# Kernel tuning notes

Hardware: AMD Instinct MI355X
Metric: run time of the kernel (lower is better)

## Reference

```python
import jax, jax.numpy as jnp
import numpy as np
from jax import lax

SQRT2 = 1.4142135623730951
NEG_SLOPE = 0.2


def _haar_kernels():
    l = np.ones((1, 2), np.float32) / np.float32(np.sqrt(2.0))
    h = l.copy()
    h[0, 0] = -h[0, 0]
    ll = l.T @ l
    lh = h.T @ l
    hl = l.T @ h
    hh = h.T @ h
    return (jnp.asarray(ll), jnp.asarray(lh), jnp.asarray(hl), jnp.asarray(hh))


def _blur_kernel():
    k = np.array([1.0, 3.0, 3.0, 1.0], np.float32)
    K = np.outer(k, k)
    K /= K.sum()
    return jnp.asarray(K)


def upfirdn2d(x, kernel, up=1, down=1, pad=(0, 0, 0, 0)):
    # x: [B,C,H,W]; depthwise FIR matching StyleGAN2 upfirdn2d semantics:
    # upsample by zero-insertion (up-1 zeros AFTER each sample), pad, true
    # convolution (kernel flipped, since lax does cross-correlation), then
    # stride-`down` decimation. Trailing zeros of torch's upsampling are
    # folded into the right/bottom pad (+up-1).
    B, C, H, W = x.shape
    px0, px1, py0, py1 = pad
    w = jnp.flip(kernel, (0, 1))[None, None].astype(x.dtype)  # [1,1,kh,kw]
    y = lax.conv_general_dilated(
        x.reshape(B * C, 1, H, W), w,
        window_strides=(down, down),
        padding=((py0, py1 + up - 1), (px0, px1 + up - 1)),
        lhs_dilation=(up, up),
        dimension_numbers=('NCHW', 'OIHW', 'NCHW'))
    return y.reshape(B, C, y.shape[2], y.shape[3])


def setup_inputs() -> dict:
    key = jax.random.key(0)
    k1, k2, k3 = jax.random.split(key, 3)
    x = jax.random.normal(k1, (8, 16, 512, 512), dtype=jnp.float32)
    conv_w = jax.random.normal(k2, (512, 16, 1, 1), dtype=jnp.float32)
    conv_b = jax.random.normal(k3, (512,), dtype=jnp.float32) * 0.1
    return {"x": x, "conv_w": conv_w, "conv_b": conv_b}


def reference(x, conv_w, conv_b):
    ll, lh, hl, hh = _haar_kernels()
    # ---- InverseHaarTransform(4): 16ch [B,16,H,W] -> 4ch [B,4,2H,2W] ----
    xll, xlh, xhl, xhh = jnp.split(x, 4, axis=1)
    p = (1, 0, 1, 0)
    inv = (upfirdn2d(xll, ll, up=2, pad=p)
           + upfirdn2d(xlh, -lh, up=2, pad=p)
           + upfirdn2d(xhl, -hl, up=2, pad=p)
           + upfirdn2d(xhh, hh, up=2, pad=p))
    # ---- Downsample(blur_kernel=[1,3,3,1]): [B,4,2H,2W] -> [B,4,H,W] ----
    bk = _blur_kernel()
    pp = bk.shape[0] - 2  # p = len(kernel) - factor
    pad0, pad1 = (pp + 1) // 2, pp // 2
    dwn = upfirdn2d(inv, bk, down=2, pad=(pad0, pad1, pad0, pad1))
    # ---- HaarTransform(4): [B,4,H,W] -> [B,16,H/2,W/2] ----
    new_in = jnp.concatenate(
        [upfirdn2d(dwn, k, down=2, pad=(0, 0, 0, 0)) for k in (ll, lh, hl, hh)],
        axis=1)
    # ---- ConvLayer: EqualConv2d 1x1 (no bias) + FusedLeakyReLU ----
    fan_in = conv_w.shape[1] * conv_w.shape[2] * conv_w.shape[3]
    scale = 1.0 / float(np.sqrt(fan_in))
    out = jnp.einsum('bchw,oc->bohw', new_in, conv_w[:, :, 0, 0] * scale)
    out = out + conv_b[None, :, None, None]
    out = jnp.where(out >= 0, out, NEG_SLOPE * out) * SQRT2
    return (new_in, out)
```

## Files before the change

kernel.cpp:

```cpp
#include <hip/hip_runtime.h>


#define H_IN 512
#define W_IN 512
#define H_OUT 256
#define W_OUT 256
#define NB 8
#define C_MID 16
#define C_OUT 512

typedef float fx4 __attribute__((ext_vector_type(4)));

__device__ __forceinline__ float cL(int fsel, float a0, float a1, float a2, float a3) {
  return fsel == 0 ? (a0 + 7.f*a1 + 7.f*a2 + a3) : (a0 + a1 - a2 - a3);
}
__device__ __forceinline__ float cH(int fsel, float a0, float a1, float a2, float a3) {
  return fsel == 0 ? (a0 + 5.f*a1 - 5.f*a2 - a3) : (a0 - a1 - a2 + a3);
}

__global__ __launch_bounds__(256) void k_stage1(const float* __restrict__ x,
                                                float* __restrict__ nin) {
  const int t  = threadIdx.x;
  const int q  = t & 63;
  const int oy = blockIdx.x * 4 + (t >> 6);
  const int bz = blockIdx.y;
  const int b = bz >> 2, ch = bz & 3;
  const int y0 = 2 * oy - 1;

  const float WL[2][4] = {{1.f, 7.f, 7.f, 1.f}, {1.f, 1.f, -1.f, -1.f}};
  const float WH[2][4] = {{1.f, 5.f, -5.f, -1.f}, {1.f, -1.f, -1.f, 1.f}};

  float acc[4][4];
#pragma unroll
  for (int i = 0; i < 4; ++i)
#pragma unroll
    for (int k = 0; k < 4; ++k) acc[i][k] = 0.f;

#pragma unroll
  for (int g = 0; g < 4; ++g) {
    const int gY = g & 1, gX = g >> 1;
    const float sg = (g == 1 || g == 2) ? -1.f : 1.f;
    const float* xp = x + (size_t)(b * 16 + g * 4 + ch) * (H_IN * W_IN);
#pragma unroll
    for (int p = 0; p < 4; ++p) {
      const int yy = y0 + p;
      if (yy < 0 || yy >= H_IN) continue;
      const float* row = xp + (size_t)yy * W_IN + 8 * q;
      float c[10];
      c[0] = (q > 0) ? row[-1] : 0.f;
      const fx4 m0 = *reinterpret_cast<const fx4*>(row);
      const fx4 m1 = *reinterpret_cast<const fx4*>(row + 4);
      c[1] = m0.x; c[2] = m0.y; c[3] = m0.z; c[4] = m0.w;
      c[5] = m1.x; c[6] = m1.y; c[7] = m1.z; c[8] = m1.w;
      c[9] = (q < 63) ? row[8] : 0.f;
      const float wl = sg * WL[gY][p];
      const float wh = sg * WH[gY][p];
#pragma unroll
      for (int xo = 0; xo < 4; ++xo) {
        const float a0 = c[2*xo], a1 = c[2*xo+1], a2 = c[2*xo+2], a3 = c[2*xo+3];
        const float vL = cL(gX, a0, a1, a2, a3);
        const float vH = cH(gX, a0, a1, a2, a3);
        acc[0][xo] = fmaf(wl, vL, acc[0][xo]);
        acc[1][xo] = fmaf(wh, vL, acc[1][xo]);
        acc[2][xo] = fmaf(wl, vH, acc[2][xo]);
        acc[3][xo] = fmaf(wh, vH, acc[3][xo]);
      }
    }
  }

  const float inv = 1.f / 256.f;
#pragma unroll
  for (int comp = 0; comp < 4; ++comp) {
    fx4 r;
    r.x = acc[comp][0] * inv; r.y = acc[comp][1] * inv;
    r.z = acc[comp][2] * inv; r.w = acc[comp][3] * inv;
    *reinterpret_cast<fx4*>(
        nin + ((size_t)(b * 16 + comp * 4 + ch) * H_OUT + oy) * W_OUT + 4 * q) = r;
  }
}

__device__ __forceinline__ fx4 vfma(fx4 v, float s, fx4 a) {
  a.x = fmaf(v.x, s, a.x); a.y = fmaf(v.y, s, a.y);
  a.z = fmaf(v.z, s, a.z); a.w = fmaf(v.w, s, a.w);
  return a;
}

__global__ __launch_bounds__(256) void k_stage2(const float* __restrict__ nin,
                                                const float* __restrict__ w,
                                                const float* __restrict__ bias,
                                                float* __restrict__ out) {
  __shared__ fx4 ws4[128 * 4];
  __shared__ float bs[128];
  const int t = threadIdx.x;
  const int chunk = blockIdx.z;
  const int obase = 128 * chunk;

  const fx4* w4 = reinterpret_cast<const fx4*>(w + (size_t)obase * 16);
  ws4[t]       = w4[t] * 0.25f;
  ws4[t + 256] = w4[t + 256] * 0.25f;
  if (t < 128) bs[t] = bias[obase + t];
  __syncthreads();

  const int by = blockIdx.x;
  const int b  = blockIdx.y;
  const int y  = 4 * by + (t >> 6);
  const int xq = (t & 63) * 4;

  const float* np = nin + ((size_t)(b * C_MID) * H_OUT + y) * W_OUT + xq;
  fx4 v[16];
#pragma unroll
  for (int c = 0; c < 16; ++c)
    v[c] = *reinterpret_cast<const fx4*>(np + (size_t)c * (H_OUT * W_OUT));

  float* op = out + ((size_t)(b * C_OUT + obase) * H_OUT + y) * W_OUT + xq;
  const float s2 = 1.41421356237309515f;
#pragma unroll 2
  for (int o = 0; o < 128; ++o) {
    const fx4 w0 = ws4[4*o], w1 = ws4[4*o+1], w2 = ws4[4*o+2], w3 = ws4[4*o+3];
    const float bo = bs[o];
    fx4 a; a.x = bo; a.y = bo; a.z = bo; a.w = bo;
    a = vfma(v[0],  w0.x, a); a = vfma(v[1],  w0.y, a);
    a = vfma(v[2],  w0.z, a); a = vfma(v[3],  w0.w, a);
    a = vfma(v[4],  w1.x, a); a = vfma(v[5],  w1.y, a);
    a = vfma(v[6],  w1.z, a); a = vfma(v[7],  w1.w, a);
    a = vfma(v[8],  w2.x, a); a = vfma(v[9],  w2.y, a);
    a = vfma(v[10], w2.z, a); a = vfma(v[11], w2.w, a);
    a = vfma(v[12], w3.x, a); a = vfma(v[13], w3.y, a);
    a = vfma(v[14], w3.z, a); a = vfma(v[15], w3.w, a);
    a.x = (a.x >= 0.f ? a.x : 0.2f * a.x) * s2;
    a.y = (a.y >= 0.f ? a.y : 0.2f * a.y) * s2;
    a.z = (a.z >= 0.f ? a.z : 0.2f * a.z) * s2;
    a.w = (a.w >= 0.f ? a.w : 0.2f * a.w) * s2;
    __builtin_nontemporal_store(a,
        reinterpret_cast<fx4*>(op + (size_t)o * (H_OUT * W_OUT)));
  }
}

extern "C" void kernel_launch(void* const* d_in, const int* in_sizes, int n_in,
                              void* d_out, int out_size, void* d_ws, size_t ws_size,
                              hipStream_t stream) {
  const float* x    = (const float*)d_in[0];
  const float* w    = (const float*)d_in[1];
  const float* bias = (const float*)d_in[2];
  float* nin = (float*)d_out;
  float* out = (float*)d_out + (size_t)NB * C_MID * H_OUT * W_OUT;

  k_stage1<<<dim3(64, 32), dim3(256), 0, stream>>>(x, nin);
  k_stage2<<<dim3(64, 8, 4), dim3(256), 0, stream>>>(nin, w, bias, out);
}
```

Before: 264.8 us.

## Fuse Haar/blur stage and 1x1 conv into single kernel keeping features in registers

Merges the wavelet/blur stage and the 1x1 conv + leaky ReLU stage into one kernel. Each thread computes all 16 mid channels for its pixels and keeps them in registers, then loops over all 512 output channels, so the intermediate no longer has to be read back from global memory and one launch is saved. In exchange the grid shrinks from 2048+2048 blocks to 512 blocks, each doing 4x more output work and holding 8KB+ of weights in LDS, which lowers parallelism and occupancy on a large GPU.

```diff
diff --git a/kernel.cpp b/kernel.cpp
--- a/kernel.cpp
+++ b/kernel.cpp
@@ -18,115 +18,104 @@
   return fsel == 0 ? (a0 + 5.f*a1 - 5.f*a2 - a3) : (a0 - a1 - a2 + a3);
 }
 
-__global__ __launch_bounds__(256) void k_stage1(const float* __restrict__ x,
-                                                float* __restrict__ nin) {
-  const int t  = threadIdx.x;
-  const int q  = t & 63;
-  const int oy = blockIdx.x * 4 + (t >> 6);
-  const int bz = blockIdx.y;
-  const int b = bz >> 2, ch = bz & 3;
-  const int y0 = 2 * oy - 1;
+__device__ __forceinline__ fx4 vfma(fx4 v, float s, fx4 a) {
+  a.x = fmaf(v.x, s, a.x); a.y = fmaf(v.y, s, a.y);
+  a.z = fmaf(v.z, s, a.z); a.w = fmaf(v.w, s, a.w);
+  return a;
+}
+
+__global__ __launch_bounds__(256) void k_fused(const float* __restrict__ x,
+                                               const float* __restrict__ w,
+                                               const float* __restrict__ bias,
+                                               float* __restrict__ nin,
+                                               float* __restrict__ out) {
+  __shared__ fx4 ws4[C_OUT * 4];
+  __shared__ float bs[C_OUT];
+  const int t = threadIdx.x;
+
+  const fx4* w4 = reinterpret_cast<const fx4*>(w);
+  const float wscale = 0.25f * (1.f / 256.f);
+#pragma unroll
+  for (int i = 0; i < 8; ++i) ws4[t + 256 * i] = w4[t + 256 * i] * wscale;
+  bs[t] = bias[t];
+  bs[t + 256] = bias[t + 256];
+
+  const int q = t & 63;
+  const int y = blockIdx.x * 4 + (t >> 6);
+  const int b = blockIdx.y;
+  const int y0 = 2 * y - 1;
 
   const float WL[2][4] = {{1.f, 7.f, 7.f, 1.f}, {1.f, 1.f, -1.f, -1.f}};
   const float WH[2][4] = {{1.f, 5.f, -5.f, -1.f}, {1.f, -1.f, -1.f, 1.f}};
 
-  float acc[4][4];
+  fx4 acc[16];
 #pragma unroll
-  for (int i = 0; i < 4; ++i)
-#pragma unroll
-    for (int k = 0; k < 4; ++k) acc[i][k] = 0.f;
+  for (int c = 0; c < 16; ++c) acc[c] = (fx4){0.f, 0.f, 0.f, 0.f};
 
 #pragma unroll
-  for (int g = 0; g < 4; ++g) {
-    const int gY = g & 1, gX = g >> 1;
-    const float sg = (g == 1 || g == 2) ? -1.f : 1.f;
-    const float* xp = x + (size_t)(b * 16 + g * 4 + ch) * (H_IN * W_IN);
+  for (int ch = 0; ch < 4; ++ch) {
 #pragma unroll
-    for (int p = 0; p < 4; ++p) {
-      const int yy = y0 + p;
-      if (yy < 0 || yy >= H_IN) continue;
-      const float* row = xp + (size_t)yy * W_IN + 8 * q;
-      float c[10];
-      c[0] = (q > 0) ? row[-1] : 0.f;
-      const fx4 m0 = *reinterpret_cast<const fx4*>(row);
-      const fx4 m1 = *reinterpret_cast<const fx4*>(row + 4);
-      c[1] = m0.x; c[2] = m0.y; c[3] = m0.z; c[4] = m0.w;
-      c[5] = m1.x; c[6] = m1.y; c[7] = m1.z; c[8] = m1.w;
-      c[9] = (q < 63) ? row[8] : 0.f;
-      const float wl = sg * WL[gY][p];
-      const float wh = sg * WH[gY][p];
+    for (int g = 0; g < 4; ++g) {
+      const int gY = g & 1, gX = g >> 1;
+      const float sg = (g == 1 || g == 2) ? -1.f : 1.f;
+      const float* xp = x + (size_t)(b * 16 + g * 4 + ch) * (H_IN * W_IN);
 #pragma unroll
-      for (int xo = 0; xo < 4; ++xo) {
-        const float a0 = c[2*xo], a1 = c[2*xo+1], a2 = c[2*xo+2], a3 = c[2*xo+3];
-        const float vL = cL(gX, a0, a1, a2, a3);
-        const float vH = cH(gX, a0, a1, a2, a3);
-        acc[0][xo] = fmaf(wl, vL, acc[0][xo]);
-        acc[1][xo] = fmaf(wh, vL, acc[1][xo]);
-        acc[2][xo] = fmaf(wl, vH, acc[2][xo]);
-        acc[3][xo] = fmaf(wh, vH, acc[3][xo]);
+      for (int p = 0; p < 4; ++p) {
+        const int yy = y0 + p;
+        if (yy < 0 || yy >= H_IN) continue;
+        const float* row = xp + (size_t)yy * W_IN + 8 * q;
+        float c0 = (q > 0) ? row[-1] : 0.f;
+        const fx4 m0 = *reinterpret_cast<const fx4*>(row);
+        const fx4 m1 = *reinterpret_cast<const fx4*>(row + 4);
+        const float c9 = (q < 63) ? row[8] : 0.f;
+        const float cc[10] = {c0, m0.x, m0.y, m0.z, m0.w,
+                              m1.x, m1.y, m1.z, m1.w, c9};
+        const float wl = sg * WL[gY][p];
+        const float wh = sg * WH[gY][p];
+        fx4 vL, vH;
+        vL.x = cL(gX, cc[0], cc[1], cc[2], cc[3]);
+        vL.y = cL(gX, cc[2], cc[3], cc[4], cc[5]);
+        vL.z = cL(gX, cc[4], cc[5], cc[6], cc[7]);
+        vL.w = cL(gX, cc[6], cc[7], cc[8], cc[9]);
+        vH.x = cH(gX, cc[0], cc[1], cc[2], cc[3]);
+        vH.y = cH(gX, cc[2], cc[3], cc[4], cc[5]);
+        vH.z = cH(gX, cc[4], cc[5], cc[6], cc[7]);
+        vH.w = cH(gX, cc[6], cc[7], cc[8], cc[9]);
+        acc[0 * 4 + ch] = vfma(vL, wl, acc[0 * 4 + ch]);
+        acc[1 * 4 + ch] = vfma(vL, wh, acc[1 * 4 + ch]);
+        acc[2 * 4 + ch] = vfma(vH, wl, acc[2 * 4 + ch]);
+        acc[3 * 4 + ch] = vfma(vH, wh, acc[3 * 4 + ch]);
       }
     }
   }
 
   const float inv = 1.f / 256.f;
 #pragma unroll
-  for (int comp = 0; comp < 4; ++comp) {
+  for (int c = 0; c < 16; ++c) {
     fx4 r;
-    r.x = acc[comp][0] * inv; r.y = acc[comp][1] * inv;
-    r.z = acc[comp][2] * inv; r.w = acc[comp][3] * inv;
+    r.x = acc[c].x * inv; r.y = acc[c].y * inv;
+    r.z = acc[c].z * inv; r.w = acc[c].w * inv;
     *reinterpret_cast<fx4*>(
-        nin + ((size_t)(b * 16 + comp * 4 + ch) * H_OUT + oy) * W_OUT + 4 * q) = r;
+        nin + ((size_t)(b * C_MID + c) * H_OUT + y) * W_OUT + 4 * q) = r;
   }
-}
 
-__device__ __forceinline__ fx4 vfma(fx4 v, float s, fx4 a) {
-  a.x = fmaf(v.x, s, a.x); a.y = fmaf(v.y, s, a.y);
-  a.z = fmaf(v.z, s, a.z); a.w = fmaf(v.w, s, a.w);
-  return a;
-}
-
-__global__ __launch_bounds__(256) void k_stage2(const float* __restrict__ nin,
-                                                const float* __restrict__ w,
-                                                const float* __restrict__ bias,
-                                                float* __restrict__ out) {
-  __shared__ fx4 ws4[128 * 4];
-  __shared__ float bs[128];
-  const int t = threadIdx.x;
-  const int chunk = blockIdx.z;
-  const int obase = 128 * chunk;
-
-  const fx4* w4 = reinterpret_cast<const fx4*>(w + (size_t)obase * 16);
-  ws4[t]       = w4[t] * 0.25f;
-  ws4[t + 256] = w4[t + 256] * 0.25f;
-  if (t < 128) bs[t] = bias[obase + t];
   __syncthreads();
 
-  const int by = blockIdx.x;
-  const int b  = blockIdx.y;
-  const int y  = 4 * by + (t >> 6);
-  const int xq = (t & 63) * 4;
-
-  const float* np = nin + ((size_t)(b * C_MID) * H_OUT + y) * W_OUT + xq;
-  fx4 v[16];
-#pragma unroll
-  for (int c = 0; c < 16; ++c)
-    v[c] = *reinterpret_cast<const fx4*>(np + (size_t)c * (H_OUT * W_OUT));
-
-  float* op = out + ((size_t)(b * C_OUT + obase) * H_OUT + y) * W_OUT + xq;
+  float* op = out + ((size_t)(b * C_OUT) * H_OUT + y) * W_OUT + 4 * q;
   const float s2 = 1.41421356237309515f;
 #pragma unroll 2
-  for (int o = 0; o < 128; ++o) {
+  for (int o = 0; o < C_OUT; ++o) {
     const fx4 w0 = ws4[4*o], w1 = ws4[4*o+1], w2 = ws4[4*o+2], w3 = ws4[4*o+3];
     const float bo = bs[o];
     fx4 a; a.x = bo; a.y = bo; a.z = bo; a.w = bo;
-    a = vfma(v[0],  w0.x, a); a = vfma(v[1],  w0.y, a);
-    a = vfma(v[2],  w0.z, a); a = vfma(v[3],  w0.w, a);
-    a = vfma(v[4],  w1.x, a); a = vfma(v[5],  w1.y, a);
-    a = vfma(v[6],  w1.z, a); a = vfma(v[7],  w1.w, a);
-    a = vfma(v[8],  w2.x, a); a = vfma(v[9],  w2.y, a);
-    a = vfma(v[10], w2.z, a); a = vfma(v[11], w2.w, a);
-    a = vfma(v[12], w3.x, a); a = vfma(v[13], w3.y, a);
-    a = vfma(v[14], w3.z, a); a = vfma(v[15], w3.w, a);
+    a = vfma(acc[0],  w0.x, a); a = vfma(acc[1],  w0.y, a);
+    a = vfma(acc[2],  w0.z, a); a = vfma(acc[3],  w0.w, a);
+    a = vfma(acc[4],  w1.x, a); a = vfma(acc[5],  w1.y, a);
+    a = vfma(acc[6],  w1.z, a); a = vfma(acc[7],  w1.w, a);
+    a = vfma(acc[8],  w2.x, a); a = vfma(acc[9],  w2.y, a);
+    a = vfma(acc[10], w2.z, a); a = vfma(acc[11], w2.w, a);
+    a = vfma(acc[12], w3.x, a); a = vfma(acc[13], w3.y, a);
+    a = vfma(acc[14], w3.z, a); a = vfma(acc[15], w3.w, a);
     a.x = (a.x >= 0.f ? a.x : 0.2f * a.x) * s2;
     a.y = (a.y >= 0.f ? a.y : 0.2f * a.y) * s2;
     a.z = (a.z >= 0.f ? a.z : 0.2f * a.z) * s2;
@@ -145,6 +134,5 @@
   float* nin = (float*)d_out;
   float* out = (float*)d_out + (size_t)NB * C_MID * H_OUT * W_OUT;
 
-  k_stage1<<<dim3(64, 32), dim3(256), 0, stream>>>(x, nin);
-  k_stage2<<<dim3(64, 8, 4), dim3(256), 0, stream>>>(nin, w, bias, out);
+  k_fused<<<dim3(64, 8), dim3(256), 0, stream>>>(x, w, bias, nin, out);
 }
```

Measured after the change: 267.5 us. Within noise of the previous version (+1.0%).
